# Performance work log

Measured on AMD Instinct MI355X. Metric: run time of the kernel, lower is better.

Reference implementation:

```python
import jax, jax.numpy as jnp
import numpy as np

C = 64
RED = 4            # attention reduction: conv_match C -> C//RED
CR = C // RED      # 16, also MultiScaleSpatialAttention reduced channels
N_HASHES = 4
CHUNK = 512
RES_SCALE = 0.1
EPS = 5e-5


def conv2d(x, w, b=None, padding=0, groups=1):
    out = jax.lax.conv_general_dilated(
        x, w, (1, 1), [(padding, padding), (padding, padding)],
        dimension_numbers=('NCHW', 'OIHW', 'NCHW'), feature_group_count=groups)
    if b is not None:
        out = out + b[None, :, None, None]
    return out


def ds_conv(x, pw_w, dw_w, dw_b, padding):
    # pointwise (no bias) then depthwise (bias)
    x = conv2d(x, pw_w)
    return conv2d(x, dw_w, dw_b, padding=padding, groups=dw_w.shape[0])


def pool2(x, mode):
    B, Cc, H, W = x.shape
    xr = x.reshape(B, Cc, H // 2, 2, W // 2, 2)
    return xr.max(axis=(3, 5)) if mode == 'max' else xr.mean(axis=(3, 5))


def bilinear_ac(x, out_h, out_w):
    # bilinear interpolation with align_corners=True (matches F.interpolate)
    B, Cc, h, w = x.shape
    def coords(n_in, n_out):
        pos = jnp.arange(n_out, dtype=x.dtype) * ((n_in - 1) / (n_out - 1))
        lo = jnp.floor(pos).astype(jnp.int32)
        hi = jnp.minimum(lo + 1, n_in - 1)
        frac = pos - lo.astype(x.dtype)
        return lo, hi, frac
    lo_h, hi_h, fh = coords(h, out_h)
    x = x[:, :, lo_h, :] * (1 - fh)[None, None, :, None] + x[:, :, hi_h, :] * fh[None, None, :, None]
    lo_w, hi_w, fw = coords(w, out_w)
    x = x[:, :, :, lo_w] * (1 - fw) + x[:, :, :, hi_w] * fw
    return x


def sparse_attn(x, wm, bm, wa, ba, rot):
    # NLSN-style LSH-chunked non-local sparse attention
    N, Cc, H, W = x.shape
    L = H * W
    xe = conv2d(x, wm, bm).reshape(N, -1, L).transpose(0, 2, 1)   # [N,L,Ce]
    ye = conv2d(x, wa, ba).reshape(N, -1, L).transpose(0, 2, 1)   # [N,L,C]
    Ce = xe.shape[-1]
    n_chunks = L // CHUNK                     # L multiple of CHUNK here -> no padding
    buckets = min(n_chunks + n_chunks % 2, 128)
    # LSH hashing (rot: [Ce, n_hashes, buckets//2])
    rv = jnp.einsum('blf,fhi->bhli', xe, rot)
    rv = jnp.concatenate([rv, -rv], axis=-1)  # [N,nh,L,buckets]
    codes = jnp.argmax(rv, axis=-1) + (jnp.arange(N_HASHES) * buckets)[None, :, None]
    codes = codes.reshape(N, -1)              # [N, nh*L]
    idx = jnp.argsort(codes, axis=-1)
    undo = jnp.argsort(idx, axis=-1)
    mod_idx = idx % L
    xs = jnp.take_along_axis(xe, mod_idx[:, :, None], axis=1)     # [N,nh*L,Ce]
    ys = jnp.take_along_axis(ye, mod_idx[:, :, None], axis=1)     # [N,nh*L,C]
    xb = xs.reshape(N, N_HASHES, n_chunks, CHUNK, Ce)
    yb = ys.reshape(N, N_HASHES, n_chunks, CHUNK, Cc)
    xm = xb / jnp.maximum(jnp.linalg.norm(xb, axis=-1, keepdims=True), EPS)
    def adj(t):  # add previous / next bucket (circular)
        return jnp.concatenate([t, jnp.roll(t, 1, axis=2), jnp.roll(t, -1, axis=2)], axis=3)
    xm3, yb3 = adj(xm), adj(yb)
    raw = jnp.einsum('bhkie,bhkje->bhkij', xb, xm3)               # [N,nh,k,CHUNK,3*CHUNK]
    bscore = jax.nn.logsumexp(raw, axis=-1, keepdims=True)
    score = jnp.exp(raw - bscore)
    ret = jnp.einsum('bhkij,bhkje->bhkie', score, yb3)            # [N,nh,k,CHUNK,C]
    ret = ret.reshape(N, N_HASHES * L, Cc)
    bscore = bscore.reshape(N, N_HASHES * L)
    ret = jnp.take_along_axis(ret, undo[:, :, None], axis=1).reshape(N, N_HASHES, L, Cc)
    bscore = jnp.take_along_axis(bscore, undo, axis=1).reshape(N, N_HASHES, L, 1)
    probs = jax.nn.softmax(bscore, axis=1)                        # over hash rounds
    out = (ret * probs).sum(axis=1)                               # [N,L,C]
    out = out.transpose(0, 2, 1).reshape(N, Cc, H, W)
    return out * RES_SCALE + x


def setup_inputs() -> dict:
    key = jax.random.key(0)
    ks = iter(jax.random.split(key, 40))
    w = lambda *s: jax.random.normal(next(ks), s, jnp.float32) * 0.1
    inp = {
        'x': jax.random.normal(next(ks), (2, C, 128, 128), jnp.float32),
        'spa_down_w': w(CR, C, 1, 1), 'spa_down_b': w(CR),
        's0_pw_w': w(2 * CR, CR, 1, 1), 's0_dw_w': w(2 * CR, 1, 1, 1), 's0_dw_b': w(2 * CR),
        'br3_pw_w': w(CR, CR, 1, 1), 'br3_dw_w': w(CR, 1, 3, 3), 'br3_dw_b': w(CR),
        'br5_pw_w': w(CR, CR, 1, 1), 'br5_dw_w': w(CR, 1, 5, 5), 'br5_dw_b': w(CR),
        'br7_pw_w': w(CR, CR, 1, 1), 'br7_dw_w': w(CR, 1, 7, 7), 'br7_dw_b': w(CR),
        'fusion_w': w(C, 8 * CR, 1, 1), 'fusion_b': w(C),
        'resid_w': w(C, C, 1, 1), 'resid_b': w(C),
        'ca_w1': w(C // 16, C, 1, 1), 'ca_b1': w(C // 16),
        'ca_w2': w(C, C // 16, 1, 1), 'ca_b2': w(C),
        'conv1x1_w': w(C, C, 1, 1), 'conv1x1_b': w(C),
        'match_w': w(CR, C, 1, 1), 'match_b': w(CR),
        'asm_w': w(C, C, 1, 1), 'asm_b': w(C),
        'rot': jax.random.normal(next(ks), (CR, N_HASHES, 16), jnp.float32),  # buckets//2 = 16
        'collect_w': w(C, C, 1, 1), 'collect_b': w(C),
    }
    return inp


def reference(x, spa_down_w, spa_down_b, s0_pw_w, s0_dw_w, s0_dw_b,
              br3_pw_w, br3_dw_w, br3_dw_b, br5_pw_w, br5_dw_w, br5_dw_b,
              br7_pw_w, br7_dw_w, br7_dw_b, fusion_w, fusion_b,
              resid_w, resid_b, ca_w1, ca_b1, ca_w2, ca_b2,
              conv1x1_w, conv1x1_b, match_w, match_b, asm_w, asm_b, rot,
              collect_w, collect_b):
    B, Cc, H, W = x.shape
    # --- MultiScaleSpatialAttention ---
    xr = conv2d(x, spa_down_w, spa_down_b)                # [B,16,H,W]
    s0 = ds_conv(xr, s0_pw_w, s0_dw_w, s0_dw_b, padding=0)
    feats = [s0]
    for pw, dw, db, pad in ((br3_pw_w, br3_dw_w, br3_dw_b, 1),
                            (br5_pw_w, br5_dw_w, br5_dw_b, 2),
                            (br7_pw_w, br7_dw_w, br7_dw_b, 3)):
        mx = ds_conv(pool2(xr, 'max'), pw, dw, db, pad)
        av = ds_conv(pool2(xr, 'avg'), pw, dw, db, pad)
        feats.append(jnp.concatenate([bilinear_ac(mx, H, W), bilinear_ac(av, H, W)], axis=1))
    attn = jax.nn.sigmoid(conv2d(jnp.concatenate(feats, axis=1), fusion_w, fusion_b))
    spa_mask = x * attn + conv2d(x, resid_w, resid_b)
    # --- CALayer ---
    y = x.mean(axis=(2, 3), keepdims=True)
    y = jax.nn.sigmoid(conv2d(jax.nn.relu(conv2d(y, ca_w1, ca_b1)), ca_w2, ca_b2))
    spe_mask = x * y
    # --- combine + SparseMaskConv (n_layers=1: attention then 1x1 collect) ---
    mask = conv2d(spa_mask + spe_mask, conv1x1_w, conv1x1_b) + x
    fea = sparse_attn(mask, match_w, match_b, asm_w, asm_b, rot)
    out1 = conv2d(fea, collect_w, collect_b)
    return out1 + x
```

## Files before the change

### kernel.cpp

```cpp
#include <hip/hip_runtime.h>
#include <math.h>

static constexpr int NB = 2;
static constexpr int NC = 64;
static constexpr int NHp = 128, NWp = 128;
static constexpr int NL = NHp * NWp;
static constexpr int NCR = 16;
static constexpr int NL2 = 64 * 64;
static constexpr int NHASH = 4;
static constexpr int CHUNKSZ = 512;
static constexpr int NCHUNKS = 32;
static constexpr int TOT = NHASH * NL;
static constexpr int NKEY = 128;
static constexpr int NTILE = 256;
static constexpr int TILESZ = TOT / NTILE;

typedef _Float16 half4 __attribute__((ext_vector_type(4)));
typedef _Float16 half8 __attribute__((ext_vector_type(8)));
typedef float f32x4 __attribute__((ext_vector_type(4)));

static constexpr size_t OFF_MASK = 0;
static constexpr size_t OFF_FEA  = OFF_MASK + (size_t)NB*NC*NL;
static constexpr size_t OFF_XE   = OFF_FEA  + (size_t)NB*NC*NL;
static constexpr size_t OFF_XEH  = OFF_XE   + (size_t)NB*NL*NCR;
static constexpr size_t OFF_XENH = OFF_XEH  + (size_t)NB*NL*NCR/2;
static constexpr size_t OFF_YEH  = OFF_XENH + (size_t)NB*NL*NCR/2;
static constexpr size_t OFF_RET  = OFF_YEH  + (size_t)NB*NL*NC/2;
static constexpr size_t OFF_BSC  = OFF_RET  + (size_t)NB*TOT*NC/2;
static constexpr size_t OFF_INT  = OFF_BSC  + (size_t)NB*TOT;
static constexpr size_t IOFF_CODES = 0;
static constexpr size_t IOFF_IDX   = IOFF_CODES + (size_t)NB*TOT;
static constexpr size_t IOFF_UNDO  = IOFF_IDX   + (size_t)NB*TOT;
static constexpr size_t IOFF_HIST  = IOFF_UNDO  + (size_t)NB*TOT;
static constexpr size_t IOFF_OFFS  = IOFF_HIST  + (size_t)NB*NKEY*NTILE/2;
static constexpr size_t IOFF_END   = IOFF_OFFS  + (size_t)NB*NKEY*NTILE/2;
static constexpr size_t OFF_CAY = OFF_INT + IOFF_END;
static constexpr size_t OFF_CAS = OFF_CAY + 128;
static constexpr size_t OFF_CRW = OFF_CAS + 128;
static constexpr size_t OFF_CRB = OFF_CRW + 4096;
static constexpr size_t OFF_PMX   = OFF_FEA;
static constexpr size_t OFF_PAV   = OFF_PMX  + (size_t)NB*NCR*NL2;
static constexpr size_t OFF_PTMP  = OFF_PAV  + (size_t)NB*NCR*NL2;
static constexpr size_t OFF_DWT   = OFF_PTMP + (size_t)6*NB*NCR*NL2;
static_assert(OFF_DWT + (size_t)6*NB*NCR*NL2 <= OFF_XE, "halfres overlay fits");
static constexpr size_t OFF_XR    = OFF_XE;
static constexpr size_t OFF_FEATS = OFF_XR + (size_t)NB*NCR*NL;
static_assert(OFF_FEATS + (size_t)NB*128*NL <= OFF_BSC, "feats overlay fits");
static constexpr size_t OFF_PRE1  = OFF_FEA;

__device__ __forceinline__ float sigmoidf_(float v){ return 1.0f/(1.0f + expf(-v)); }


__global__ __launch_bounds__(256,4) void k_xr(const float* __restrict__ x,
                     const float* __restrict__ w,
                     const float* __restrict__ b, float* __restrict__ xr){
  int gid = blockIdx.x*256 + threadIdx.x;
  int pix = gid >> 1, hf = gid & 1;
  int bb = pix >> 14, p = pix & (NL-1);
  const float* xi = x + (size_t)bb*NC*NL + (size_t)hf*32*NL + p;
  float acc[16];
  #pragma unroll
  for (int oc=0; oc<16; ++oc) acc[oc] = hf ? 0.f : b[oc];
  for (int ic0=0; ic0<32; ic0+=16){
    float r[16];
    #pragma unroll
    for (int j=0; j<16; ++j) r[j] = xi[(size_t)(ic0+j)*NL];
    #pragma unroll
    for (int oc=0; oc<16; ++oc){
      #pragma unroll
      for (int j=0; j<16; ++j) acc[oc] += r[j]*w[oc*64 + hf*32 + ic0 + j];
    }
  }
  #pragma unroll
  for (int oc=0; oc<16; ++oc) acc[oc] += __shfl_xor(acc[oc], 1, 64);
  if (!hf){
    float* xo = xr + (size_t)bb*NCR*NL + p;
    #pragma unroll
    for (int oc=0; oc<16; ++oc) xo[(size_t)oc*NL] = acc[oc];
  }
}

__global__ __launch_bounds__(256,4) void k_s0(const float* __restrict__ xr,
                     const float* __restrict__ pw,
                     const float* __restrict__ dww, const float* __restrict__ dwb,
                     float* __restrict__ feats){
  int gid = blockIdx.x*256 + threadIdx.x;
  int oc0 = blockIdx.y*16;
  int bb = gid >> 14, p = gid & (NL-1);
  const float* xi = xr + (size_t)bb*NCR*NL + p;
  float r[16];
  #pragma unroll
  for (int ic=0; ic<16; ++ic) r[ic] = xi[(size_t)ic*NL];
  float* fo = feats + (size_t)bb*128*NL + p;
  #pragma unroll
  for (int j=0; j<16; ++j){
    int oc = oc0 + j;
    float s = 0.f;
    #pragma unroll
    for (int ic=0; ic<16; ++ic) s += r[ic]*pw[oc*16+ic];
    fo[(size_t)oc*NL] = s*dww[oc] + dwb[oc];
  }
}

__global__ void k_pool(const float* __restrict__ xr, float* __restrict__ pmax,
                       float* __restrict__ pavg){
  int gid = blockIdx.x*256 + threadIdx.x;
  if (gid >= NB*NCR*NL2) return;
  int p = gid & (NL2-1); int t = gid >> 12; int c = t & 15; int bb = t >> 4;
  int y = p >> 6, x2 = p & 63;
  const float* base = xr + (size_t)(bb*NCR + c)*NL + (size_t)(2*y)*NWp + 2*x2;
  float a = base[0], b_ = base[1], c_ = base[NWp], d = base[NWp+1];
  pmax[gid] = fmaxf(fmaxf(a,b_), fmaxf(c_,d));
  pavg[gid] = 0.25f*(a+b_+c_+d);
}

__global__ void k_pw16_all(const float* __restrict__ pmx, const float* __restrict__ pav,
                           const float* __restrict__ w0, const float* __restrict__ w1,
                           const float* __restrict__ w2, float* __restrict__ out){
  int gid = blockIdx.x*256 + threadIdx.x;
  if (gid >= 6*NB*NL2) return;
  int p = gid & (NL2-1); int t = gid >> 12; int bb = t & 1; int combo = t >> 1;
  int br = combo >> 1, mode = combo & 1;
  const float* w = (br==0) ? w0 : (br==1) ? w1 : w2;
  const float* in = ((mode==0) ? pmx : pav) + (size_t)bb*NCR*NL2 + p;
  float r[16];
  #pragma unroll
  for (int ic=0; ic<16; ++ic) r[ic] = in[(size_t)ic*NL2];
  float* oo = out + ((size_t)(combo*NB + bb)*NCR)*NL2 + p;
  #pragma unroll
  for (int oc=0; oc<16; ++oc){
    float s = 0.f;
    #pragma unroll
    for (int ic=0; ic<16; ++ic) s += r[ic]*w[oc*16+ic];
    oo[(size_t)oc*NL2] = s;
  }
}

__global__ void k_dw_all(const float* __restrict__ in,
                         const float* __restrict__ w3, const float* __restrict__ b3,
                         const float* __restrict__ w5, const float* __restrict__ b5,
                         const float* __restrict__ w7, const float* __restrict__ b7,
                         float* __restrict__ out){
  int gid = blockIdx.x*256 + threadIdx.x;
  if (gid >= 6*NB*NCR*NL2) return;
  int p = gid & (NL2-1); int t = gid >> 12; int c = t & 15; int r2 = t >> 4;
  int bb = r2 & 1; int combo = r2 >> 1;
  int br = combo >> 1;
  int K = (br==0) ? 3 : (br==1) ? 5 : 7; int P = K >> 1;
  const float* w = (br==0) ? w3 : (br==1) ? w5 : w7;
  const float* bias = (br==0) ? b3 : (br==1) ? b5 : b7;
  int y = p >> 6, x = p & 63;
  const float* xi = in + ((size_t)(combo*NB + bb)*NCR + c)*NL2;
  float s = bias[c];
  for (int dy=0; dy<K; ++dy){
    int iy = y + dy - P;
    if ((unsigned)iy < 64u){
      for (int dx=0; dx<K; ++dx){
        int ix = x + dx - P;
        if ((unsigned)ix < 64u) s += xi[iy*64 + ix] * w[(c*K + dy)*K + dx];
      }
    }
  }
  out[gid] = s;
}

__global__ void k_up_all(const float* __restrict__ in, float* __restrict__ feats){
  int gid = blockIdx.x*256 + threadIdx.x;
  if (gid >= 6*NB*NCR*NL) return;
  int p = gid & (NL-1); int t = gid >> 14; int c = t & 15; int r2 = t >> 4;
  int bb = r2 & 1; int combo = r2 >> 1;
  int y = p >> 7, x = p & 127;
  const float sc = 63.0f/127.0f;
  float fy = y*sc; int ly = (int)floorf(fy); int hy = min(ly+1, 63); fy -= (float)ly;
  float fx = x*sc; int lx = (int)floorf(fx); int hx = min(lx+1, 63); float gx = fx - (float)lx;
  const float* xi = in + ((size_t)(combo*NB + bb)*NCR + c)*NL2;
  float v0 = xi[ly*64+lx]*(1.f-fy) + xi[hy*64+lx]*fy;
  float v1 = xi[ly*64+hx]*(1.f-fy) + xi[hy*64+hx]*fy;
  int coff = 32 + combo*16 + c;
  feats[(size_t)bb*128*NL + (size_t)coff*NL + p] = v0*(1.f-gx) + v1*gx;
}

__global__ void k_camean(const float* __restrict__ x, float* __restrict__ cay){
  __shared__ float red[256];
  int bc = blockIdx.x; int tid = threadIdx.x;
  float s = 0.f;
  for (int i = tid; i < NL; i += 256) s += x[(size_t)bc*NL + i];
  red[tid] = s; __syncthreads();
  for (int st=128; st>0; st>>=1){ if (tid<st) red[tid]+=red[tid+st]; __syncthreads(); }
  if (tid==0) cay[bc] = red[0] / (float)NL;
}

__global__ void k_camlp(const float* __restrict__ cay,
                        const float* __restrict__ w1, const float* __restrict__ b1,
                        const float* __restrict__ w2, const float* __restrict__ b2,
                        float* __restrict__ cas){
  __shared__ float z[NB*4];
  int tid = threadIdx.x;
  if (tid < NB*4){
    int bb = tid >> 2, j = tid & 3;
    float s = b1[j];
    for (int ic=0; ic<NC; ++ic) s += cay[bb*NC+ic]*w1[j*NC+ic];
    z[tid] = fmaxf(s, 0.f);
  }
  __syncthreads();
  if (tid < NB*NC){
    int bb = tid >> 6, oc = tid & 63;
    float s = b2[oc];
    #pragma unroll
    for (int j=0; j<4; ++j) s += z[bb*4+j]*w2[oc*4+j];
    cas[tid] = sigmoidf_(s);
  }
}

__global__ void k_wprod(const float* __restrict__ c11w, const float* __restrict__ c11b,
                        const float* __restrict__ rw, const float* __restrict__ rb,
                        float* __restrict__ crw, float* __restrict__ crb){
  int gid = blockIdx.x*256 + threadIdx.x;
  if (gid >= 4096) return;
  int o = gid >> 6, i = gid & 63;
  float s = 0.f;
  for (int k=0; k<64; ++k) s += c11w[o*64+k]*rw[k*64+i];
  crw[gid] = s;
  if (i == 0){
    float t = c11b[o];
    for (int k=0; k<64; ++k) t += c11w[o*64+k]*rb[k];
    crb[o] = t;
  }
}

__global__ __launch_bounds__(256,4) void k_attnmul(const float* __restrict__ x,
                          const float* __restrict__ feats,
                          const float* __restrict__ fw, const float* __restrict__ fb,
                          const float* __restrict__ cas, float* __restrict__ pre1){
  int gid = blockIdx.x*256 + threadIdx.x;
  int oc0 = blockIdx.y*16;
  int bb = gid >> 14, p = gid & (NL-1);
  const float* fi = feats + (size_t)bb*128*NL + p;
  float acc[16];
  #pragma unroll
  for (int j=0; j<16; ++j) acc[j] = fb[oc0+j];
  for (int k0=0; k0<128; k0+=8){
    float fr[8];
    #pragma unroll
    for (int j=0; j<8; ++j) fr[j] = fi[(size_t)(k0+j)*NL];
    #pragma unroll
    for (int j=0; j<16; ++j){
      #pragma unroll
      for (int t=0; t<8; ++t) acc[j] += fr[t]*fw[(oc0+j)*128+k0+t];
    }
  }
  const float* xb = x + (size_t)bb*NC*NL + p;
  float* po = pre1 + (size_t)bb*NC*NL + p;
  #pragma unroll
  for (int j=0; j<16; ++j){
    int oc = oc0 + j;
    float xv = xb[(size_t)oc*NL];
    po[(size_t)oc*NL] = xv*(sigmoidf_(acc[j]) + cas[bb*64+oc]);
  }
}

__global__ __launch_bounds__(256,4) void k_mask(const float* __restrict__ pre1,
                       const float* __restrict__ c11w,
                       const float* __restrict__ crw, const float* __restrict__ crb,
                       const float* __restrict__ x, float* __restrict__ mask){
  int gid = blockIdx.x*256 + threadIdx.x;
  int oc0 = blockIdx.y*16;
  int bb = gid >> 14, p = gid & (NL-1);
  const float* pi = pre1 + (size_t)bb*NC*NL + p;
  const float* xi = x + (size_t)bb*NC*NL + p;
  float acc[16];
  #pragma unroll
  for (int j=0; j<16; ++j) acc[j] = crb[oc0+j];
  for (int ic0=0; ic0<64; ic0+=8){
    float pr[8], xr8[8];
    #pragma unroll
    for (int j=0; j<8; ++j){ pr[j] = pi[(size_t)(ic0+j)*NL]; xr8[j] = xi[(size_t)(ic0+j)*NL]; }
    #pragma unroll
    for (int j=0; j<16; ++j){
      #pragma unroll
      for (int t=0; t<8; ++t)
        acc[j] += pr[t]*c11w[(oc0+j)*64+ic0+t] + xr8[t]*crw[(oc0+j)*64+ic0+t];
    }
  }
  float* mo = mask + (size_t)bb*NC*NL + p;
  #pragma unroll
  for (int j=0; j<16; ++j){
    int oc = oc0 + j;
    mo[(size_t)oc*NL] = acc[j] + xi[(size_t)oc*NL];
  }
}


__global__ __launch_bounds__(256,4) void k_xe(const float* __restrict__ mask,
                     const float* __restrict__ w, const float* __restrict__ b,
                     const float* __restrict__ rot,
                     _Float16* __restrict__ xeh, _Float16* __restrict__ xenh,
                     int* __restrict__ codes){
  int gid = blockIdx.x*256 + threadIdx.x;
  int pix = gid >> 1, hf = gid & 1;
  int bb = pix >> 14, l = pix & (NL-1);
  const float* mi = mask + (size_t)bb*NC*NL + (size_t)hf*32*NL + l;
  float acc[16];
  #pragma unroll
  for (int oc=0; oc<16; ++oc) acc[oc] = hf ? 0.f : b[oc];
  for (int ic0=0; ic0<32; ic0+=16){
    float r[16];
    #pragma unroll
    for (int j=0; j<16; ++j) r[j] = mi[(size_t)(ic0+j)*NL];
    #pragma unroll
    for (int oc=0; oc<16; ++oc){
      #pragma unroll
      for (int j=0; j<16; ++j) acc[oc] += r[j]*w[oc*64 + hf*32 + ic0 + j];
    }
  }
  #pragma unroll
  for (int oc=0; oc<16; ++oc) acc[oc] += __shfl_xor(acc[oc], 1, 64);
  if (!hf){
    float n2 = 0.f;
    #pragma unroll
    for (int oc=0; oc<16; ++oc) n2 += acc[oc]*acc[oc];
    float inv = 1.0f / fmaxf(sqrtf(n2), 5e-5f);
    _Float16* ho = xeh + (size_t)pix*NCR;
    _Float16* no = xenh + (size_t)pix*NCR;
    #pragma unroll
    for (int g=0; g<4; ++g){
      half4 hv, nv;
      #pragma unroll
      for (int j=0; j<4; ++j){ hv[j] = (_Float16)acc[g*4+j]; nv[j] = (_Float16)(acc[g*4+j]*inv); }
      *(half4*)(ho + g*4) = hv;
      *(half4*)(no + g*4) = nv;
    }
  }
  #pragma unroll
  for (int hh=0; hh<2; ++hh){
    int h = hf*2 + hh;
    float rv[16];
    #pragma unroll
    for (int i=0; i<16; ++i){
      float s = 0.f;
      #pragma unroll
      for (int f=0; f<16; ++f) s += acc[f]*rot[(f*NHASH + h)*16 + i];
      rv[i] = s;
    }
    float best = -1e30f; int bi = 0;
    #pragma unroll
    for (int i=0; i<16; ++i){ if (rv[i] > best){ best = rv[i]; bi = i; } }
    #pragma unroll
    for (int i=0; i<16; ++i){ float val = -rv[i]; if (val > best){ best = val; bi = 16+i; } }
    codes[((bb*NHASH + h) << 14) + l] = bi + h*32;
  }
}

__global__ __launch_bounds__(256,4) void k_yeh(const float* __restrict__ mask,
                      const float* __restrict__ w,
                      const float* __restrict__ b, _Float16* __restrict__ yeh){
  int gid = blockIdx.x*256 + threadIdx.x;
  int oc0 = blockIdx.y*16;
  int bb = gid >> 14, l = gid & (NL-1);
  const float* mi = mask + (size_t)bb*NC*NL + l;
  float acc[16];
  #pragma unroll
  for (int j=0; j<16; ++j) acc[j] = b[oc0+j];
  for (int ic0=0; ic0<64; ic0+=8){
    float r[8];
    #pragma unroll
    for (int j=0; j<8; ++j) r[j] = mi[(size_t)(ic0+j)*NL];
    #pragma unroll
    for (int j=0; j<16; ++j){
      #pragma unroll
      for (int t=0; t<8; ++t) acc[j] += r[t]*w[(oc0+j)*64+ic0+t];
    }
  }
  _Float16* yo = yeh + (size_t)(bb*NL + l)*NC + oc0;
  #pragma unroll
  for (int g=0; g<2; ++g){
    half8 h;
    #pragma unroll
    for (int j=0; j<8; ++j) h[j] = (_Float16)acc[g*8+j];
    *(half8*)(yo + g*8) = h;
  }
}

__global__ void k_hist(const int* __restrict__ codes, int* __restrict__ hist){
  __shared__ int h[NKEY];
  int bt = blockIdx.x; int bb = bt >> 8; int tile = bt & 255;
  int tid = threadIdx.x;
  h[tid] = 0; __syncthreads();
  for (int i = tid; i < TILESZ; i += 128)
    atomicAdd(&h[codes[bb*TOT + tile*TILESZ + i]], 1);
  __syncthreads();
  hist[bb*NKEY*NTILE + tid*NTILE + tile] = h[tid];
}

__global__ void k_scan(const int* __restrict__ hist, int* __restrict__ offs){
  __shared__ int part[256];
  int bb = blockIdx.x; int t = threadIdx.x;
  const int* hi = hist + (size_t)bb*NKEY*NTILE;
  int* oo = offs + (size_t)bb*NKEY*NTILE;
  int s = 0;
  for (int i=0; i<128; ++i) s += hi[t*128 + i];
  part[t] = s; __syncthreads();
  if (t == 0){ int acc = 0; for (int i=0;i<256;++i){ int v=part[i]; part[i]=acc; acc+=v; } }
  __syncthreads();
  int run = part[t];
  for (int i=0; i<128; ++i){ int v = hi[t*128+i]; oo[t*128+i] = run; run += v; }
}

__global__ void k_scatter(const int* __restrict__ codes, const int* __restrict__ offs,
                          int* __restrict__ idx, int* __restrict__ undo){
  __shared__ int cnt[NKEY];
  int tid = threadIdx.x;
  cnt[tid] = 0; __syncthreads();
  if (tid == 0){
    int bt = blockIdx.x; int bb = bt >> 8; int tile = bt & 255;
    const int* cb = codes + bb*TOT;
    const int* ob = offs + (size_t)bb*NKEY*NTILE;
    int* ib = idx + bb*TOT;
    int* ub = undo + bb*TOT;
    #pragma unroll 4
    for (int i=0; i<TILESZ; ++i){
      int j = tile*TILESZ + i;
      int k = cb[j];
      int pos = ob[k*NTILE + tile] + cnt[k]++;
      ib[pos] = j;
      ub[j] = pos;
    }
  }
}

__global__ __launch_bounds__(512) void k_attn(
    const _Float16* __restrict__ xeh, const _Float16* __restrict__ xenh,
    const _Float16* __restrict__ yeh, const int* __restrict__ idx,
    _Float16* __restrict__ retb, float* __restrict__ bsc){
  __shared__ _Float16 kt[64*24];
  __shared__ _Float16 vt[64*72];
  int blk = blockIdx.x;
  int qh = blk & 1; int kk = (blk >> 1) & 31; int h = (blk >> 6) & 3; int bb = blk >> 8;
  int tid = threadIdx.x;
  int w = tid >> 6, lane = tid & 63, col = lane & 15, grp = lane >> 4;
  const int* idxb = idx + bb*TOT;
  int qbase = h*NL + kk*CHUNKSZ + qh*256 + w*32;

  half4 qfr[2]; int posq[2];
  #pragma unroll
  for (int qf=0; qf<2; ++qf){
    posq[qf] = qbase + qf*16 + col;
    int lq = idxb[posq[qf]] & (NL-1);
    qfr[qf] = *(const half4*)(xeh + ((size_t)bb*NL + lq)*16 + grp*4);
  }

  f32x4 O[4][2];
  #pragma unroll
  for (int a=0; a<4; ++a)
    #pragma unroll
    for (int b=0; b<2; ++b) O[a][b] = (f32x4){0.f,0.f,0.f,0.f};
  float m_[2] = {-1e30f,-1e30f};
  float ssum[2] = {0.f,0.f};

  for (int t=0; t<24; ++t){
    __syncthreads();
    {
      int kx = tid & 63, c0 = (tid >> 6) * 8;
      int jj = t*64 + kx; int sec = jj >> 9; int j0 = jj & 511;
      int cc = kk + ((sec==1) ? -1 : (sec==2) ? 1 : 0);
      cc = (cc + NCHUNKS) & (NCHUNKS-1);
      int lv = idxb[h*NL + cc*CHUNKSZ + j0] & (NL-1);
      half8 vv = *(const half8*)(yeh + ((size_t)bb*NL + lv)*64 + c0);
      #pragma unroll
      for (int j=0; j<8; ++j) vt[(c0+j)*72 + kx] = vv[j];
    }
    if (tid < 128){
      int r = tid >> 1, hf = tid & 1;
      int jj = t*64 + r; int sec = jj >> 9; int j0 = jj & 511;
      int cc = kk + ((sec==1) ? -1 : (sec==2) ? 1 : 0);
      cc = (cc + NCHUNKS) & (NCHUNKS-1);
      int lk = idxb[h*NL + cc*CHUNKSZ + j0] & (NL-1);
      *(half8*)(kt + r*24 + hf*8) =
          *(const half8*)(xenh + ((size_t)bb*NL + lk)*16 + hf*8);
    }
    __syncthreads();

    f32x4 S[4][2];
    #pragma unroll
    for (int kb=0; kb<4; ++kb){
      half4 ka = *(const half4*)(kt + (kb*16 + col)*24 + grp*4);
      #pragma unroll
      for (int qf=0; qf<2; ++qf)
        S[kb][qf] = __builtin_amdgcn_mfma_f32_16x16x16f16(
            ka, qfr[qf], (f32x4){0.f,0.f,0.f,0.f}, 0, 0, 0);
    }

    half4 pf[2][4];
    #pragma unroll
    for (int qf=0; qf<2; ++qf){
      float mt = -1e30f;
      #pragma unroll
      for (int kb=0; kb<4; ++kb)
        #pragma unroll
        for (int i=0; i<4; ++i) mt = fmaxf(mt, S[kb][qf][i]);
      mt = fmaxf(mt, __shfl_xor(mt, 16, 64));
      mt = fmaxf(mt, __shfl_xor(mt, 32, 64));
      if (__any(mt > m_[qf] + 8.0f)){
        float mn = fmaxf(m_[qf], mt);
        float sc = __expf(m_[qf] - mn);
        ssum[qf] *= sc;
        m_[qf] = mn;
        #pragma unroll
        for (int cf=0; cf<4; ++cf)
          #pragma unroll
          for (int i=0; i<4; ++i) O[cf][qf][i] *= sc;
      }
      float ps = 0.f;
      #pragma unroll
      for (int kb=0; kb<4; ++kb){
        #pragma unroll
        for (int i=0; i<4; ++i){
          float p = __expf(S[kb][qf][i] - m_[qf]);
          ps += p;
          pf[qf][kb][i] = (_Float16)p;
        }
      }
      ps += __shfl_xor(ps, 16, 64);
      ps += __shfl_xor(ps, 32, 64);
      ssum[qf] += ps;
    }

    #pragma unroll
    for (int cf=0; cf<4; ++cf){
      #pragma unroll
      for (int kb=0; kb<4; ++kb){
        half4 va = *(const half4*)(vt + (cf*16 + col)*72 + kb*16 + grp*4);
        #pragma unroll
        for (int qf=0; qf<2; ++qf)
          O[cf][qf] = __builtin_amdgcn_mfma_f32_16x16x16f16(
              va, pf[qf][kb], O[cf][qf], 0, 0, 0);
      }
    }
  }

  #pragma unroll
  for (int qf=0; qf<2; ++qf){
    float inv = 1.0f/ssum[qf];
    size_t rb = ((size_t)bb*TOT + posq[qf])*64;
    #pragma unroll
    for (int cf=0; cf<4; ++cf){
      half4 o;
      #pragma unroll
      for (int i=0; i<4; ++i) o[i] = (_Float16)(O[cf][qf][i]*inv);
      *(half4*)(retb + rb + cf*16 + grp*4) = o;
    }
    if (grp == 0) bsc[(size_t)bb*TOT + posq[qf]] = m_[qf] + logf(ssum[qf]);
  }
}

__global__ __launch_bounds__(256,4) void k_combine(const _Float16* __restrict__ retb,
                          const float* __restrict__ bsc,
                          const int* __restrict__ undo, const float* __restrict__ mask,
                          float* __restrict__ fea){
  int gid = blockIdx.x*256 + threadIdx.x;
  int c0 = blockIdx.y*32;
  int bb = gid >> 14; int l = gid & (NL-1);
  const int* ub = undo + bb*TOT;
  int pos[4]; float sc[4];
  #pragma unroll
  for (int h=0; h<4; ++h){ pos[h] = ub[h*NL + l]; sc[h] = bsc[bb*TOT + pos[h]]; }
  float mx = fmaxf(fmaxf(sc[0],sc[1]), fmaxf(sc[2],sc[3]));
  float e[4]; float tot = 0.f;
  #pragma unroll
  for (int h=0; h<4; ++h){ e[h] = __expf(sc[h]-mx); tot += e[h]; }
  float inv = 0.1f/tot;
  const float* mb_ = mask + (size_t)bb*NC*NL + l;
  float* fo = fea + (size_t)bb*NC*NL + l;
  const _Float16* r0 = retb + ((size_t)bb*TOT + pos[0])*NC + c0;
  const _Float16* r1 = retb + ((size_t)bb*TOT + pos[1])*NC + c0;
  const _Float16* r2 = retb + ((size_t)bb*TOT + pos[2])*NC + c0;
  const _Float16* r3 = retb + ((size_t)bb*TOT + pos[3])*NC + c0;
  #pragma unroll
  for (int g=0; g<4; ++g){
    half8 v0 = *(const half8*)(r0 + g*8);
    half8 v1 = *(const half8*)(r1 + g*8);
    half8 v2 = *(const half8*)(r2 + g*8);
    half8 v3 = *(const half8*)(r3 + g*8);
    #pragma unroll
    for (int j=0; j<8; ++j){
      int c = c0 + g*8 + j;
      float v = (float)v0[j]*e[0] + (float)v1[j]*e[1] + (float)v2[j]*e[2] + (float)v3[j]*e[3];
      fo[(size_t)c*NL] = v*inv + mb_[(size_t)c*NL];
    }
  }
}

__global__ __launch_bounds__(256,4) void k_collect(const float* __restrict__ fea,
                          const float* __restrict__ w,
                          const float* __restrict__ b, const float* __restrict__ x,
                          float* __restrict__ out){
  int gid = blockIdx.x*256 + threadIdx.x;
  int oc0 = blockIdx.y*16;
  int bb = gid >> 14, p = gid & (NL-1);
  const float* fi = fea + (size_t)bb*NC*NL + p;
  const float* xi = x + (size_t)bb*NC*NL + p;
  float acc[16];
  #pragma unroll
  for (int j=0; j<16; ++j) acc[j] = b[oc0+j];
  for (int ic0=0; ic0<64; ic0+=8){
    float r[8];
    #pragma unroll
    for (int j=0; j<8; ++j) r[j] = fi[(size_t)(ic0+j)*NL];
    #pragma unroll
    for (int j=0; j<16; ++j){
      #pragma unroll
      for (int t=0; t<8; ++t) acc[j] += r[t]*w[(oc0+j)*64+ic0+t];
    }
  }
  float* oo = out + (size_t)bb*NC*NL + p;
  #pragma unroll
  for (int j=0; j<16; ++j){
    int oc = oc0 + j;
    oo[(size_t)oc*NL] = acc[j] + xi[(size_t)oc*NL];
  }
}

extern "C" void kernel_launch(void* const* d_in, const int* in_sizes, int n_in,
                              void* d_out, int out_size, void* d_ws, size_t ws_size,
                              hipStream_t stream) {
  const float* x        = (const float*)d_in[0];
  const float* spa_dw   = (const float*)d_in[1];
  const float* spa_db   = (const float*)d_in[2];
  const float* s0_pw    = (const float*)d_in[3];
  const float* s0_dww   = (const float*)d_in[4];
  const float* s0_dwb   = (const float*)d_in[5];
  const float* fus_w    = (const float*)d_in[15];
  const float* fus_b    = (const float*)d_in[16];
  const float* res_w    = (const float*)d_in[17];
  const float* res_b    = (const float*)d_in[18];
  const float* ca_w1    = (const float*)d_in[19];
  const float* ca_b1    = (const float*)d_in[20];
  const float* ca_w2    = (const float*)d_in[21];
  const float* ca_b2    = (const float*)d_in[22];
  const float* c11_w    = (const float*)d_in[23];
  const float* c11_b    = (const float*)d_in[24];
  const float* match_w  = (const float*)d_in[25];
  const float* match_b  = (const float*)d_in[26];
  const float* asm_w    = (const float*)d_in[27];
  const float* asm_b    = (const float*)d_in[28];
  const float* rot      = (const float*)d_in[29];
  const float* col_w    = (const float*)d_in[30];
  const float* col_b    = (const float*)d_in[31];
  float* out = (float*)d_out;

  float* ws    = (float*)d_ws;
  float* mask  = ws + OFF_MASK;
  float* fea   = ws + OFF_FEA;
  _Float16* xeh  = (_Float16*)(ws + OFF_XEH);
  _Float16* xenh = (_Float16*)(ws + OFF_XENH);
  _Float16* yeh  = (_Float16*)(ws + OFF_YEH);
  _Float16* retb = (_Float16*)(ws + OFF_RET);
  float* bsc   = ws + OFF_BSC;
  int*   ib    = (int*)(ws + OFF_INT);
  int* codes   = ib + IOFF_CODES;
  int* idx     = ib + IOFF_IDX;
  int* undo    = ib + IOFF_UNDO;
  int* hist    = ib + IOFF_HIST;
  int* offs    = ib + IOFF_OFFS;
  float* cay   = ws + OFF_CAY;
  float* cas   = ws + OFF_CAS;
  float* crw   = ws + OFF_CRW;
  float* crb   = ws + OFF_CRB;
  float* xr    = ws + OFF_XR;
  float* feats = ws + OFF_FEATS;
  float* pmx   = ws + OFF_PMX;
  float* pav   = ws + OFF_PAV;
  float* ptmp  = ws + OFF_PTMP;
  float* dwt   = ws + OFF_DWT;
  float* pre1  = ws + OFF_PRE1;

  k_xr<<<(NB*NL*2)/256, 256, 0, stream>>>(x, spa_dw, spa_db, xr);
  k_wprod<<<16, 256, 0, stream>>>(c11_w, c11_b, res_w, res_b, crw, crb);
  k_s0<<<dim3((NB*NL)/256, 2), 256, 0, stream>>>(xr, s0_pw, s0_dww, s0_dwb, feats);
  k_pool<<<(NB*NCR*NL2)/256, 256, 0, stream>>>(xr, pmx, pav);
  k_pw16_all<<<(6*NB*NL2)/256, 256, 0, stream>>>(pmx, pav,
      (const float*)d_in[6], (const float*)d_in[9], (const float*)d_in[12], ptmp);
  k_dw_all<<<(6*NB*NCR*NL2)/256, 256, 0, stream>>>(ptmp,
      (const float*)d_in[7], (const float*)d_in[8],
      (const float*)d_in[10], (const float*)d_in[11],
      (const float*)d_in[13], (const float*)d_in[14], dwt);
  k_up_all<<<(6*NB*NCR*NL)/256, 256, 0, stream>>>(dwt, feats);
  k_camean<<<NB*NC, 256, 0, stream>>>(x, cay);
  k_camlp<<<1, 128, 0, stream>>>(cay, ca_w1, ca_b1, ca_w2, ca_b2, cas);
  k_attnmul<<<dim3((NB*NL)/256, 4), 256, 0, stream>>>(x, feats, fus_w, fus_b, cas, pre1);
  k_mask<<<dim3((NB*NL)/256, 4), 256, 0, stream>>>(pre1, c11_w, crw, crb, x, mask);

  k_xe<<<(NB*NL*2)/256, 256, 0, stream>>>(mask, match_w, match_b, rot, xeh, xenh, codes);
  k_yeh<<<dim3((NB*NL)/256, 4), 256, 0, stream>>>(mask, asm_w, asm_b, yeh);
  k_hist<<<NB*NTILE, 128, 0, stream>>>(codes, hist);
  k_scan<<<NB, 256, 0, stream>>>(hist, offs);
  k_scatter<<<NB*NTILE, 128, 0, stream>>>(codes, offs, idx, undo);
  k_attn<<<NB*NHASH*NCHUNKS*2, 512, 0, stream>>>(xeh, xenh, yeh, idx, retb, bsc);
  k_combine<<<dim3((NB*NL)/256, 2), 256, 0, stream>>>(retb, bsc, undo, mask, fea);
  k_collect<<<dim3((NB*NL)/256, 4), 256, 0, stream>>>(fea, col_w, col_b, x, out);
}
```

Before: 327.1 us.

## Fuse histogram into hashing, parallelize scan and scatter, split attention blocks finer

The histogram is now built with global atomics inside the LSH hashing kernel after a memset, which removes the separate k_hist pass. The block scan is now a parallel Hillis-Steele scan, and the scatter now uses one wavefront per tile with ballot-based match ranking, replacing the single-thread serial loop. The attention kernel processes one 16-query fragment per wave with twice as many blocks, reduces row sums only once at the end, and pads V in shared memory to stride 70. These changes trade more global atomics and more K/V reloads across blocks for much more parallelism in the sort stages and more blocks in attention.

```diff
diff --git a/kernel.cpp b/kernel.cpp
--- a/kernel.cpp
+++ b/kernel.cpp
@@ -295,7 +295,7 @@
                      const float* __restrict__ w, const float* __restrict__ b,
                      const float* __restrict__ rot,
                      _Float16* __restrict__ xeh, _Float16* __restrict__ xenh,
-                     int* __restrict__ codes){
+                     int* __restrict__ codes, int* __restrict__ hist){
   int gid = blockIdx.x*256 + threadIdx.x;
   int pix = gid >> 1, hf = gid & 1;
   int bb = pix >> 14, l = pix & (NL-1);
@@ -347,7 +347,10 @@
     for (int i=0; i<16; ++i){ if (rv[i] > best){ best = rv[i]; bi = i; } }
     #pragma unroll
     for (int i=0; i<16; ++i){ float val = -rv[i]; if (val > best){ best = val; bi = 16+i; } }
-    codes[((bb*NHASH + h) << 14) + l] = bi + h*32;
+    int code = bi + h*32;
+    codes[((bb*NHASH + h) << 14) + l] = code;
+    int tile = h*64 + (l >> 8);
+    atomicAdd(&hist[bb*NKEY*NTILE + code*NTILE + tile], 1);
   }
 }
 
@@ -379,17 +382,6 @@
     for (int j=0; j<8; ++j) h[j] = (_Float16)acc[g*8+j];
     *(half8*)(yo + g*8) = h;
   }
-}
-
-__global__ void k_hist(const int* __restrict__ codes, int* __restrict__ hist){
-  __shared__ int h[NKEY];
-  int bt = blockIdx.x; int bb = bt >> 8; int tile = bt & 255;
-  int tid = threadIdx.x;
-  h[tid] = 0; __syncthreads();
-  for (int i = tid; i < TILESZ; i += 128)
-    atomicAdd(&h[codes[bb*TOT + tile*TILESZ + i]], 1);
-  __syncthreads();
-  hist[bb*NKEY*NTILE + tid*NTILE + tile] = h[tid];
 }
 
 __global__ void k_scan(const int* __restrict__ hist, int* __restrict__ offs){
@@ -400,31 +392,51 @@
   int s = 0;
   for (int i=0; i<128; ++i) s += hi[t*128 + i];
   part[t] = s; __syncthreads();
-  if (t == 0){ int acc = 0; for (int i=0;i<256;++i){ int v=part[i]; part[i]=acc; acc+=v; } }
-  __syncthreads();
-  int run = part[t];
-  for (int i=0; i<128; ++i){ int v = hi[t*128+i]; oo[t*128+i] = run; run += v; }
-}
-
-__global__ void k_scatter(const int* __restrict__ codes, const int* __restrict__ offs,
+  int v = s;
+  for (int off=1; off<256; off<<=1){
+    int u = (t >= off) ? part[t-off] : 0;
+    __syncthreads();
+    v += u; part[t] = v;
+    __syncthreads();
+  }
+  int run = v - s;
+  for (int i=0; i<128; ++i){ int q = hi[t*128+i]; oo[t*128+i] = run; run += q; }
+}
+
+__global__ __launch_bounds__(256) void k_scatter(const int* __restrict__ codes,
+                          const int* __restrict__ offs,
                           int* __restrict__ idx, int* __restrict__ undo){
-  __shared__ int cnt[NKEY];
-  int tid = threadIdx.x;
-  cnt[tid] = 0; __syncthreads();
-  if (tid == 0){
-    int bt = blockIdx.x; int bb = bt >> 8; int tile = bt & 255;
-    const int* cb = codes + bb*TOT;
-    const int* ob = offs + (size_t)bb*NKEY*NTILE;
-    int* ib = idx + bb*TOT;
-    int* ub = undo + bb*TOT;
-    #pragma unroll 4
-    for (int i=0; i<TILESZ; ++i){
-      int j = tile*TILESZ + i;
-      int k = cb[j];
-      int pos = ob[k*NTILE + tile] + cnt[k]++;
-      ib[pos] = j;
-      ub[j] = pos;
-    }
+  __shared__ int cnt[4][NKEY];
+  int wid = threadIdx.x >> 6, lane = threadIdx.x & 63;
+  int t4 = blockIdx.x;
+  int bb = t4 >> 6;
+  int tile = (t4 & 63)*4 + wid;
+  cnt[wid][lane] = 0; cnt[wid][64+lane] = 0;
+  const int* cb = codes + bb*TOT;
+  const int* ob = offs + (size_t)bb*NKEY*NTILE;
+  int* ib = idx + bb*TOT;
+  int* ub = undo + bb*TOT;
+  for (int g=0; g<4; ++g){
+    int j = tile*TILESZ + g*64 + lane;
+    int k = cb[j];
+    unsigned long long m = ~0ull;
+    #pragma unroll
+    for (int bit=0; bit<7; ++bit){
+      unsigned long long bmask = __ballot((k >> bit) & 1);
+      m &= ((k >> bit) & 1) ? bmask : ~bmask;
+    }
+    int rank = __popcll(m & ((1ull << lane) - 1ull));
+    int leader = __ffsll((unsigned long long)m) - 1;
+    int base = 0;
+    if (lane == leader){
+      base = cnt[wid][k];
+      cnt[wid][k] = base + __popcll(m);
+    }
+    base = __shfl(base, leader, 64);
+    int pos = ob[k*NTILE + tile] + base + rank;
+    ib[pos] = j;
+    ub[j] = pos;
+    __threadfence_block();
   }
 }
 
@@ -433,29 +445,20 @@
     const _Float16* __restrict__ yeh, const int* __restrict__ idx,
     _Float16* __restrict__ retb, float* __restrict__ bsc){
   __shared__ _Float16 kt[64*24];
-  __shared__ _Float16 vt[64*72];
+  __shared__ _Float16 vt[64*70];
   int blk = blockIdx.x;
-  int qh = blk & 1; int kk = (blk >> 1) & 31; int h = (blk >> 6) & 3; int bb = blk >> 8;
+  int qq = blk & 3; int kk = (blk >> 2) & 31; int h = (blk >> 7) & 3; int bb = blk >> 9;
   int tid = threadIdx.x;
   int w = tid >> 6, lane = tid & 63, col = lane & 15, grp = lane >> 4;
   const int* idxb = idx + bb*TOT;
-  int qbase = h*NL + kk*CHUNKSZ + qh*256 + w*32;
-
-  half4 qfr[2]; int posq[2];
-  #pragma unroll
-  for (int qf=0; qf<2; ++qf){
-    posq[qf] = qbase + qf*16 + col;
-    int lq = idxb[posq[qf]] & (NL-1);
-    qfr[qf] = *(const half4*)(xeh + ((size_t)bb*NL + lq)*16 + grp*4);
-  }
-
-  f32x4 O[4][2];
-  #pragma unroll
-  for (int a=0; a<4; ++a)
-    #pragma unroll
-    for (int b=0; b<2; ++b) O[a][b] = (f32x4){0.f,0.f,0.f,0.f};
-  float m_[2] = {-1e30f,-1e30f};
-  float ssum[2] = {0.f,0.f};
+  int posq = h*NL + kk*CHUNKSZ + qq*128 + w*16 + col;
+  int lq = idxb[posq] & (NL-1);
+  half4 qfr = *(const half4*)(xeh + ((size_t)bb*NL + lq)*16 + grp*4);
+
+  f32x4 O[4];
+  #pragma unroll
+  for (int a=0; a<4; ++a) O[a] = (f32x4){0.f,0.f,0.f,0.f};
+  float m_ = -1e30f, ssum = 0.f;
 
   for (int t=0; t<24; ++t){
     __syncthreads();
@@ -467,7 +470,7 @@
       int lv = idxb[h*NL + cc*CHUNKSZ + j0] & (NL-1);
       half8 vv = *(const half8*)(yeh + ((size_t)bb*NL + lv)*64 + c0);
       #pragma unroll
-      for (int j=0; j<8; ++j) vt[(c0+j)*72 + kx] = vv[j];
+      for (int j=0; j<8; ++j) vt[(c0+j)*70 + kx] = vv[j];
     }
     if (tid < 128){
       int r = tid >> 1, hf = tid & 1;
@@ -480,77 +483,67 @@
     }
     __syncthreads();
 
-    f32x4 S[4][2];
+    f32x4 S[4];
     #pragma unroll
     for (int kb=0; kb<4; ++kb){
       half4 ka = *(const half4*)(kt + (kb*16 + col)*24 + grp*4);
-      #pragma unroll
-      for (int qf=0; qf<2; ++qf)
-        S[kb][qf] = __builtin_amdgcn_mfma_f32_16x16x16f16(
-            ka, qfr[qf], (f32x4){0.f,0.f,0.f,0.f}, 0, 0, 0);
-    }
-
-    half4 pf[2][4];
-    #pragma unroll
-    for (int qf=0; qf<2; ++qf){
-      float mt = -1e30f;
-      #pragma unroll
-      for (int kb=0; kb<4; ++kb)
+      S[kb] = __builtin_amdgcn_mfma_f32_16x16x16f16(
+          ka, qfr, (f32x4){0.f,0.f,0.f,0.f}, 0, 0, 0);
+    }
+
+    float mtl = -1e30f;
+    #pragma unroll
+    for (int kb=0; kb<4; ++kb)
+      #pragma unroll
+      for (int i=0; i<4; ++i) mtl = fmaxf(mtl, S[kb][i]);
+    if (__any(mtl > m_ + 8.0f)){
+      float mt = fmaxf(mtl, __shfl_xor(mtl, 16, 64));
+      mt = fmaxf(mt, __shfl_xor(mt, 32, 64));
+      float mn = fmaxf(m_, mt);
+      float sc = __expf(m_ - mn);
+      ssum *= sc;
+      m_ = mn;
+      #pragma unroll
+      for (int cf=0; cf<4; ++cf)
         #pragma unroll
-        for (int i=0; i<4; ++i) mt = fmaxf(mt, S[kb][qf][i]);
-      mt = fmaxf(mt, __shfl_xor(mt, 16, 64));
-      mt = fmaxf(mt, __shfl_xor(mt, 32, 64));
-      if (__any(mt > m_[qf] + 8.0f)){
-        float mn = fmaxf(m_[qf], mt);
-        float sc = __expf(m_[qf] - mn);
-        ssum[qf] *= sc;
-        m_[qf] = mn;
-        #pragma unroll
-        for (int cf=0; cf<4; ++cf)
-          #pragma unroll
-          for (int i=0; i<4; ++i) O[cf][qf][i] *= sc;
+        for (int i=0; i<4; ++i) O[cf][i] *= sc;
+    }
+    half4 pf[4];
+    float ps = 0.f;
+    #pragma unroll
+    for (int kb=0; kb<4; ++kb){
+      #pragma unroll
+      for (int i=0; i<4; ++i){
+        float p = __expf(S[kb][i] - m_);
+        ps += p;
+        pf[kb][i] = (_Float16)p;
       }
-      float ps = 0.f;
+    }
+    ssum += ps;
+
+    #pragma unroll
+    for (int cf=0; cf<4; ++cf){
       #pragma unroll
       for (int kb=0; kb<4; ++kb){
-        #pragma unroll
-        for (int i=0; i<4; ++i){
-          float p = __expf(S[kb][qf][i] - m_[qf]);
-          ps += p;
-          pf[qf][kb][i] = (_Float16)p;
-        }
+        half4 va = *(const half4*)(vt + (cf*16 + col)*70 + kb*16 + grp*4);
+        O[cf] = __builtin_amdgcn_mfma_f32_16x16x16f16(
+            va, pf[kb], O[cf], 0, 0, 0);
       }
-      ps += __shfl_xor(ps, 16, 64);
-      ps += __shfl_xor(ps, 32, 64);
-      ssum[qf] += ps;
-    }
-
-    #pragma unroll
-    for (int cf=0; cf<4; ++cf){
-      #pragma unroll
-      for (int kb=0; kb<4; ++kb){
-        half4 va = *(const half4*)(vt + (cf*16 + col)*72 + kb*16 + grp*4);
-        #pragma unroll
-        for (int qf=0; qf<2; ++qf)
-          O[cf][qf] = __builtin_amdgcn_mfma_f32_16x16x16f16(
-              va, pf[qf][kb], O[cf][qf], 0, 0, 0);
-      }
-    }
-  }
-
-  #pragma unroll
-  for (int qf=0; qf<2; ++qf){
-    float inv = 1.0f/ssum[qf];
-    size_t rb = ((size_t)bb*TOT + posq[qf])*64;
-    #pragma unroll
-    for (int cf=0; cf<4; ++cf){
-      half4 o;
-      #pragma unroll
-      for (int i=0; i<4; ++i) o[i] = (_Float16)(O[cf][qf][i]*inv);
-      *(half4*)(retb + rb + cf*16 + grp*4) = o;
-    }
-    if (grp == 0) bsc[(size_t)bb*TOT + posq[qf]] = m_[qf] + logf(ssum[qf]);
-  }
+    }
+  }
+
+  ssum += __shfl_xor(ssum, 16, 64);
+  ssum += __shfl_xor(ssum, 32, 64);
+  float inv = 1.0f/ssum;
+  size_t rb = ((size_t)bb*TOT + posq)*64;
+  #pragma unroll
+  for (int cf=0; cf<4; ++cf){
+    half4 o;
+    #pragma unroll
+    for (int i=0; i<4; ++i) o[i] = (_Float16)(O[cf][i]*inv);
+    *(half4*)(retb + rb + cf*16 + grp*4) = o;
+  }
+  if (grp == 0) bsc[(size_t)bb*TOT + posq] = m_ + logf(ssum);
 }
 
 __global__ __launch_bounds__(256,4) void k_combine(const _Float16* __restrict__ retb,
@@ -690,12 +683,12 @@
   k_attnmul<<<dim3((NB*NL)/256, 4), 256, 0, stream>>>(x, feats, fus_w, fus_b, cas, pre1);
   k_mask<<<dim3((NB*NL)/256, 4), 256, 0, stream>>>(pre1, c11_w, crw, crb, x, mask);
 
-  k_xe<<<(NB*NL*2)/256, 256, 0, stream>>>(mask, match_w, match_b, rot, xeh, xenh, codes);
+  hipMemsetAsync(hist, 0, (size_t)NB*NKEY*NTILE*sizeof(int), stream);
+  k_xe<<<(NB*NL*2)/256, 256, 0, stream>>>(mask, match_w, match_b, rot, xeh, xenh, codes, hist);
   k_yeh<<<dim3((NB*NL)/256, 4), 256, 0, stream>>>(mask, asm_w, asm_b, yeh);
-  k_hist<<<NB*NTILE, 128, 0, stream>>>(codes, hist);
   k_scan<<<NB, 256, 0, stream>>>(hist, offs);
-  k_scatter<<<NB*NTILE, 128, 0, stream>>>(codes, offs, idx, undo);
-  k_attn<<<NB*NHASH*NCHUNKS*2, 512, 0, stream>>>(xeh, xenh, yeh, idx, retb, bsc);
+  k_scatter<<<NB*NTILE/4, 256, 0, stream>>>(codes, offs, idx, undo);
+  k_attn<<<NB*NHASH*NCHUNKS*4, 512, 0, stream>>>(xeh, xenh, yeh, idx, retb, bsc);
   k_combine<<<dim3((NB*NL)/256, 2), 256, 0, stream>>>(retb, bsc, undo, mask, fea);
   k_collect<<<dim3((NB*NL)/256, 4), 256, 0, stream>>>(fea, col_w, col_b, x, out);
 }
```

Result: slower. 361.2 us (+10.4%).
